# Performance work log

Hardware: AMD Instinct MI355X
Metric: run time of the kernel (lower is better)

Reference implementation:

```python
import jax, jax.numpy as jnp
import numpy as np

B, S, D = 24, 512, 512
H, HS, HSEL = 8, 1, 2
DK = D // H
DFF = 2048
NQ, NPID = 1000, 5000
NB = 2
NL = 3 * NB  # blocks_1 (NB) + blocks_2 (2*NB)
FC1, FC2 = 512, 256


def setup_inputs():
    key = jax.random.key(0)
    ks = jax.random.split(key, 32)
    def w(k, shape, scale=0.02):
        return jax.random.normal(k, shape, dtype=jnp.float32) * scale
    inp = {}
    inp['q_data'] = jax.random.randint(ks[0], (B, S), 0, NQ + 1)
    inp['target'] = jax.random.randint(ks[1], (B, S), 0, 2)
    inp['pid_data'] = jax.random.randint(ks[2], (B, S), 0, NPID + 1)
    # embedding tables (padding_idx=0 -> zero row)
    inp['q_embed_tab'] = w(ks[3], (NQ + 1, D)).at[0].set(0.0)
    inp['qa_embed_tab'] = w(ks[4], (3, D)).at[0].set(0.0)
    inp['q_diff_tab'] = w(ks[5], (NQ + 1, D)).at[0].set(0.0)
    inp['qa_diff_tab'] = w(ks[6], (2 * NQ + 1, D)).at[0].set(0.0)
    inp['pid_diff_tab'] = w(ks[7], (NPID + 1, 1)).at[0].set(0.0)
    # stacked per-layer transformer params, leading dim NL
    inp['Wq'] = w(ks[8], (NL, D, D)); inp['bq'] = jnp.zeros((NL, D), jnp.float32)
    inp['Wv'] = w(ks[9], (NL, D, D)); inp['bv'] = jnp.zeros((NL, D), jnp.float32)
    inp['Wg'] = w(ks[10], (NL, D, H - HS))  # router, no bias
    inp['Wo'] = w(ks[11], (NL, D, D)); inp['bo'] = jnp.zeros((NL, D), jnp.float32)
    inp['ln1_g'] = jnp.ones((NL, D), jnp.float32); inp['ln1_b'] = jnp.zeros((NL, D), jnp.float32)
    inp['W1'] = w(ks[12], (NL, D, DFF)); inp['b1'] = jnp.zeros((NL, DFF), jnp.float32)
    inp['W2'] = w(ks[13], (NL, DFF, D)); inp['b2'] = jnp.zeros((NL, D), jnp.float32)
    inp['ln2_g'] = jnp.ones((NL, D), jnp.float32); inp['ln2_b'] = jnp.zeros((NL, D), jnp.float32)
    # output MLP
    inp['ow1'] = w(ks[14], (2 * D, FC1)); inp['ob1'] = jnp.zeros((FC1,), jnp.float32)
    inp['ow2'] = w(ks[15], (FC1, FC2)); inp['ob2'] = jnp.zeros((FC2,), jnp.float32)
    inp['ow3'] = w(ks[16], (FC2, 1)); inp['ob3'] = jnp.zeros((1,), jnp.float32)
    return inp


def _ln(x, g, b, eps=1e-5):
    m = x.mean(-1, keepdims=True)
    v = ((x - m) ** 2).mean(-1, keepdims=True)
    return (x - m) * jax.lax.rsqrt(v + eps) * g + b


def _moh_attn(xq, xv, strict, Wq, bq, Wv, bv, Wg, Wo, bo):
    b, s, d = xq.shape
    ql = xq @ Wq + bq            # [b,s,D]; kq_same=True so k == q
    vl = xv @ Wv + bv
    q = ql.reshape(b, s, H, DK).transpose(0, 2, 1, 3)   # [b,H,s,dk]
    v = vl.reshape(b, s, H, DK).transpose(0, 2, 1, 3)
    scores = jnp.einsum('bhid,bhjd->bhij', q, q) / np.float32(np.sqrt(DK))
    i = jnp.arange(s)[:, None]
    j = jnp.arange(s)[None, :]
    allowed = (j < i) if strict else (j <= i)
    scores = jnp.where(allowed, scores, jnp.float32(-1e9))
    scores = scores.at[:, :, 0, :].set(0.0)  # pad_zero row -> uniform softmax
    # dynamic per-token head routing on the query projection
    gates = jax.nn.softmax(ql @ Wg, axis=-1)             # [b,s,H-HS]
    idx = jax.lax.top_k(gates, HSEL)[1]                  # [b,s,HSEL]
    dyn_mask = jax.nn.one_hot(idx, H - HS, dtype=gates.dtype).sum(-2)
    dyn_scores = gates * dyn_mask
    rmask = jnp.concatenate([jnp.ones((b, s, HS), gates.dtype), dyn_scores], -1).mean(1)  # [b,H]
    attn = jax.nn.softmax(scores, axis=-1)
    ctx = jnp.einsum('bhij,bhjd->bhid', attn, v) * rmask[:, :, None, None]
    ctx = ctx.transpose(0, 2, 1, 3).reshape(b, s, d)
    return ctx @ Wo + bo


def _block(xq, xv, strict, p):
    a = _moh_attn(xq, xv, strict, *p[:7])
    x = _ln(xq + a, p[7], p[8])
    f = jnp.maximum(x @ p[9] + p[10], 0.0) @ p[11] + p[12]
    return _ln(x + f, p[13], p[14])


def reference(q_data, target, pid_data, q_embed_tab, qa_embed_tab, q_diff_tab,
              qa_diff_tab, pid_diff_tab, Wq, bq, Wv, bv, Wg, Wo, bo,
              ln1_g, ln1_b, W1, b1, W2, b2, ln2_g, ln2_b,
              ow1, ob1, ow2, ob2, ow3, ob3):
    # Rasch-style embeddings (separate_qa=False, n_pid>0)
    q_emb = q_embed_tab[q_data]
    qa_emb = qa_embed_tab[target] + q_emb
    pid_emb = pid_diff_tab[pid_data]          # [B,S,1]
    qd = q_diff_tab[q_data]
    q_emb = q_emb + pid_emb * qd
    qa_emb = qa_emb + pid_emb * (qa_diff_tab[target] + qd)
    stacks = (Wq, bq, Wv, bv, Wg, Wo, bo, ln1_g, ln1_b, W1, b1, W2, b2, ln2_g, ln2_b)
    def P(i):
        return tuple(a[i] for a in stacks)
    y, x = qa_emb, q_emb
    for i in range(NB):                       # blocks_1: mask=1 (causal incl self)
        y = _block(y, y, False, P(i))
    flag = True
    for jj in range(2 * NB):                  # blocks_2: alternate self / cross-with-y
        i = NB + jj
        if flag:
            x = _block(x, x, False, P(i)); flag = False
        else:
            x = _block(x, y, True, P(i)); flag = True
    h = jnp.concatenate([x, q_emb], -1)       # [B,S,2D]
    h = jnp.maximum(h @ ow1 + ob1, 0.0)
    h = jnp.maximum(h @ ow2 + ob2, 0.0)
    return jax.nn.sigmoid((h @ ow3 + ob3)[..., 0])  # [B,S]
```

## Files before the change

### kernel.cpp

```cpp
#include <hip/hip_runtime.h>
#include <math.h>

typedef unsigned short u16;
typedef unsigned int   u32;
typedef __attribute__((ext_vector_type(8))) short short8;
typedef __attribute__((ext_vector_type(4))) float f32x4;

#define Bb 24
#define Ss 512
#define Dd 512
#define DFFf 2048

__device__ __forceinline__ u16 f2b(float f) {
  u32 u = __float_as_uint(f);
  u32 r = (u + 0x7fffu + ((u >> 16) & 1u)) >> 16;
  return (u16)r;
}
__device__ __forceinline__ float b2f(u32 h) { return __uint_as_float(h << 16); }
__device__ __forceinline__ void cvt8(uint4 p, float* d) {
  d[0]=b2f(p.x&0xffffu); d[1]=b2f(p.x>>16);
  d[2]=b2f(p.y&0xffffu); d[3]=b2f(p.y>>16);
  d[4]=b2f(p.z&0xffffu); d[5]=b2f(p.z>>16);
  d[6]=b2f(p.w&0xffffu); d[7]=b2f(p.w>>16);
}

__global__ __launch_bounds__(256) void trans_kernel(
    const float* __restrict__ src, u16* __restrict__ dst, int K, int N,
    int dstLayer, int rowBase)
{
  __shared__ float t[32][33];
  int n0 = blockIdx.x*32, k0 = blockIdx.y*32;
  const float* s = src + (size_t)blockIdx.z*K*N;
  u16* d = dst + (size_t)blockIdx.z*dstLayer;
  int c = threadIdx.x & 31, r = threadIdx.x >> 5;
  #pragma unroll
  for (int rr=r; rr<32; rr+=8) t[rr][c] = s[(size_t)(k0+rr)*N + n0 + c];
  __syncthreads();
  #pragma unroll
  for (int rr=r; rr<32; rr+=8) d[(size_t)(rowBase + n0+rr)*K + k0 + c] = f2b(t[c][rr]);
}

__global__ __launch_bounds__(256) void embed_kernel(
    const int* __restrict__ q_data, const int* __restrict__ target, const int* __restrict__ pid_data,
    const float* __restrict__ q_tab, const float* __restrict__ qa_tab,
    const float* __restrict__ qd_tab, const float* __restrict__ qad_tab,
    const float* __restrict__ pid_tab,
    float* __restrict__ xb, float* __restrict__ yb,
    u16* __restrict__ qebf, u16* __restrict__ ybf)
{
  int t = blockIdx.x;
  int qi = q_data[t], tg = target[t], pi = pid_data[t];
  float pd = pid_tab[pi];
  const float* qe  = q_tab  + (size_t)qi*Dd;
  const float* qa  = qa_tab + (size_t)tg*Dd;
  const float* qd  = qd_tab + (size_t)qi*Dd;
  const float* qad = qad_tab+ (size_t)tg*Dd;
  size_t base = (size_t)t*Dd;
  for (int d = threadIdx.x; d < Dd; d += 256) {
    float e = qe[d], dv = qd[d];
    float qv  = e + pd*dv;
    float qav = qa[d] + e + pd*(qad[d] + dv);
    xb[base+d] = qv;  qebf[base+d] = f2b(qv);
    yb[base+d] = qav; ybf[base+d]  = f2b(qav);
  }
}

__global__ __launch_bounds__(256) void embed_x_kernel(
    const int* __restrict__ q_data, const int* __restrict__ pid_data,
    const float* __restrict__ q_tab, const float* __restrict__ qd_tab,
    const float* __restrict__ pid_tab, float* __restrict__ xb)
{
  int t = blockIdx.x;
  int qi = q_data[t], pi = pid_data[t];
  float pd = pid_tab[pi];
  const float* qe = q_tab + (size_t)qi*Dd;
  const float* qd = qd_tab + (size_t)qi*Dd;
  size_t base = (size_t)t*Dd;
  for (int d = threadIdx.x; d < Dd; d += 256)
    xb[base+d] = qe[d] + pd*qd[d];
}

__global__ __launch_bounds__(256) void gemm_bf16_kernel(
    const u16* __restrict__ A, const u16* __restrict__ A2,
    const u16* __restrict__ Wt,
    const float* __restrict__ bias, const float* __restrict__ bias2,
    float* __restrict__ Cf, u16* __restrict__ Cb, u16* __restrict__ Cb2,
    int M, int N, int K, int ldA, int ldw, int act, int nsplit, float* rinit)
{
  __shared__ u16 As[2][128*32];
  __shared__ u16 Bs[2][128*32];
  if (rinit && blockIdx.x==0 && blockIdx.y==0 && threadIdx.x < 192)
    rinit[threadIdx.x] = ((threadIdx.x & 7)==0) ? 1.f : 0.f;
  int bm = blockIdx.y*128, bn = blockIdx.x*128;
  int wv = threadIdx.x >> 6, lane = threadIdx.x & 63;
  int wm = (wv & 1)*64, wn = (wv >> 1)*64;

  const char* gAa[2]; const char* gAb[2]; const char* gB[2];
  u32 ldsOff[2];
  #pragma unroll
  for (int t=0; t<2; t++) {
    int flat = wv*128 + t*64 + lane;
    int row = flat >> 2, cb = (flat & 3)*16;
    gAa[t] = (const char*)A + ((size_t)(bm+row)*ldA)*2 + cb;
    gAb[t] = A2 ? ((const char*)A2 + ((size_t)(bm+row)*ldA)*2 + cb) : gAa[t];
    gB[t]  = (const char*)Wt + ((size_t)(bn+row)*ldw)*2 + cb;
    ldsOff[t] = (u32)(wv*128 + t*64)*16;
  }
  int selLim = A2 ? 512 : 0x7fffffff;
  int kmask  = A2 ? 511 : 0x7fffffff;

  f32x4 acc[4][4];
  #pragma unroll
  for (int i=0;i<4;i++)
    #pragma unroll
    for (int j=0;j<4;j++) acc[i][j] = (f32x4){0.f,0.f,0.f,0.f};

  int mrow = lane & 15, quad = lane >> 4;

  auto stage = [&](int kt, int buf) {
    int k0 = kt*32;
    size_t offA = (size_t)(k0 & kmask)*2;
    size_t offB = (size_t)k0*2;
    #pragma unroll
    for (int t=0; t<2; t++) {
      const char* sa = ((k0 < selLim) ? gAa[t] : gAb[t]) + offA;
      __builtin_amdgcn_global_load_lds(
          (const __attribute__((address_space(1))) void*)sa,
          (__attribute__((address_space(3))) void*)((char*)As[buf] + ldsOff[t]), 16, 0, 0);
      __builtin_amdgcn_global_load_lds(
          (const __attribute__((address_space(1))) void*)(gB[t] + offB),
          (__attribute__((address_space(3))) void*)((char*)Bs[buf] + ldsOff[t]), 16, 0, 0);
    }
  };

  int nk = K >> 5;
  stage(0, 0);
  for (int t=0; t<nk; t++) {
    __syncthreads();
    if (t+1 < nk) stage(t+1, (t+1)&1);
    const u16* Ab = As[t&1];
    const u16* Bbuf = Bs[t&1];
    short8 af[4], bfr[4];
    #pragma unroll
    for (int i=0;i<4;i++) {
      af[i]  = *(const short8*)(Ab   + (wm + i*16 + mrow)*32 + quad*8);
      bfr[i] = *(const short8*)(Bbuf + (wn + i*16 + mrow)*32 + quad*8);
    }
    #pragma unroll
    for (int i=0;i<4;i++)
      #pragma unroll
      for (int j=0;j<4;j++)
        acc[i][j] = __builtin_amdgcn_mfma_f32_16x16x32_bf16(af[i], bfr[j], acc[i][j], 0, 0, 0);
  }

  int hi = (bias2 != nullptr) && (bn >= nsplit);
  const float* bse = hi ? bias2 : bias;
  u16* outb = hi ? Cb2 : Cb;
  int cb0 = hi ? nsplit : 0;
  int strideOut = bias2 ? nsplit : N;

  #pragma unroll
  for (int i=0;i<4;i++) {
    #pragma unroll
    for (int r=0;r<4;r++) {
      int row = bm + wm + i*16 + quad*4 + r;
      #pragma unroll
      for (int j=0;j<4;j++) {
        int col = bn + wn + j*16 + mrow;
        float v = acc[i][j][r];
        if (bse) v += bse[col - cb0];
        if (act) v = fmaxf(v, 0.f);
        if (Cf)   Cf[(size_t)row*strideOut + col - cb0] = v;
        if (outb) outb[(size_t)row*strideOut + col - cb0] = f2b(v);
      }
    }
  }
}

__device__ __forceinline__ float blockSum256(float v) {
  __shared__ float sh[4];
  #pragma unroll
  for (int o=32;o;o>>=1) v += __shfl_down(v,o);
  if ((threadIdx.x & 63)==0) sh[threadIdx.x>>6]=v;
  __syncthreads();
  float r = sh[0]+sh[1]+sh[2]+sh[3];
  __syncthreads();
  return r;
}

__global__ __launch_bounds__(256) void add_ln_kernel(
    const float* __restrict__ xa, const u16* __restrict__ xbb,
    const float* __restrict__ g, const float* __restrict__ bta,
    float* __restrict__ outf, u16* __restrict__ outb)
{
  size_t base = (size_t)blockIdx.x*Dd;
  int tid = threadIdx.x;
  float v0 = xa[base+tid]     + b2f(xbb[base+tid]);
  float v1 = xa[base+tid+256] + b2f(xbb[base+tid+256]);
  float mean = blockSum256(v0+v1) * (1.f/512.f);
  float d0 = v0-mean, d1 = v1-mean;
  float var = blockSum256(d0*d0 + d1*d1) * (1.f/512.f);
  float inv = rsqrtf(var + 1e-5f);
  float r0 = d0*inv*g[tid]     + bta[tid];
  float r1 = d1*inv*g[tid+256] + bta[tid+256];
  outf[base+tid]     = r0; outb[base+tid]     = f2b(r0);
  outf[base+tid+256] = r1; outb[base+tid+256] = f2b(r1);
}

__global__ __launch_bounds__(64) void router_kernel(
    const u16* __restrict__ ql, const float* __restrict__ Wg, float* __restrict__ rmask)
{
  int b = blockIdx.x >> 3, seg = blockIdx.x & 7;
  int lane = threadIdx.x;
  int s = seg*64 + lane;
  const u16* q = ql + ((size_t)b*Ss + s)*Dd;
  float lg[7];
  #pragma unroll
  for (int k=0;k<7;k++) lg[k]=0.f;
  for (int d0=0; d0<Dd; d0+=8) {
    uint4 p = *(const uint4*)(q+d0);
    float qa[8]; cvt8(p, qa);
    #pragma unroll
    for (int i=0;i<8;i++)
      #pragma unroll
      for (int k=0;k<7;k++) lg[k] += qa[i]*Wg[(d0+i)*7+k];
  }
  float mx = lg[0];
  #pragma unroll
  for (int k=1;k<7;k++) mx = fmaxf(mx, lg[k]);
  float sum = 0.f, gt[7];
  #pragma unroll
  for (int k=0;k<7;k++){ gt[k]=__expf(lg[k]-mx); sum+=gt[k]; }
  float invs = 1.f/sum;
  #pragma unroll
  for (int k=0;k<7;k++) gt[k]*=invs;
  int i1=0; float v1=gt[0];
  #pragma unroll
  for (int k=1;k<7;k++) if (gt[k]>v1){v1=gt[k]; i1=k;}
  int i2=-1; float v2=-1e30f;
  #pragma unroll
  for (int k=0;k<7;k++) if (k!=i1 && gt[k]>v2){v2=gt[k]; i2=k;}
  #pragma unroll
  for (int k=0;k<7;k++) {
    float d = (k==i1 || k==i2) ? gt[k] : 0.f;
    #pragma unroll
    for (int o=32;o;o>>=1) d += __shfl_down(d,o);
    if (lane==0) atomicAdd(&rmask[b*8 + 1 + k], d * (1.f/512.f));
  }
}

__global__ __launch_bounds__(256) void attn_mfma_kernel(
    const u16* __restrict__ ql, const u16* __restrict__ vl,
    const float* __restrict__ rmask, u16* __restrict__ ctx, int strict)
{
  __shared__ u16 Ks[64*64];
  __shared__ u16 Vts[64*64];
  __shared__ u16 Pw[4][32*72];
  int qt = blockIdx.x;
  int b = blockIdx.y >> 3, h = blockIdx.y & 7;
  int tid = threadIdx.x;
  int wv = tid >> 6, lane = tid & 63;
  int mrow = lane & 15, quad = lane >> 4;

  int rowbase[2];
  rowbase[0] = qt*128 + wv*16;
  rowbase[1] = rowbase[0] + 64;

  short8 qf[2][2];
  #pragma unroll
  for (int i=0;i<2;i++)
    #pragma unroll
    for (int kf=0;kf<2;kf++)
      qf[i][kf] = *(const short8*)(ql + (size_t)(b*Ss + rowbase[i] + mrow)*Dd + h*64 + kf*32 + quad*8);

  f32x4 O[2][4];
  f32x4 L[2];
  #pragma unroll
  for (int i=0;i<2;i++) {
    L[i] = (f32x4){0.f,0.f,0.f,0.f};
    #pragma unroll
    for (int df=0;df<4;df++) O[i][df] = (f32x4){0.f,0.f,0.f,0.f};
  }
  short8 ones;
  #pragma unroll
  for (int z=0;z<8;z++) ones[z] = (short)0x3F80;

  int nt = 2*qt + 2;
  for (int t=0; t<nt; t++) {
    int j0 = t*64;
    __syncthreads();
    #pragma unroll
    for (int s2=0; s2<2; s2++) {
      int c = s2*256 + tid;
      int r = c >> 3, o = c & 7;
      uint4 kq = *(const uint4*)(ql + (size_t)(b*Ss + j0 + r)*Dd + h*64 + o*8);
      *(uint4*)(Ks + r*64 + ((o ^ (r&7))*8)) = kq;
    }
    {
      int j = tid & 63, d0 = (tid >> 6) * 16;
      const u16* vp = vl + (size_t)(b*Ss + j0 + j)*Dd + h*64 + d0;
      uint4 va = *(const uint4*)vp;
      uint4 vb = *(const uint4*)(vp + 8);
      u16 vals[16];
      vals[0]=(u16)va.x;  vals[1]=(u16)(va.x>>16);
      vals[2]=(u16)va.y;  vals[3]=(u16)(va.y>>16);
      vals[4]=(u16)va.z;  vals[5]=(u16)(va.z>>16);
      vals[6]=(u16)va.w;  vals[7]=(u16)(va.w>>16);
      vals[8]=(u16)vb.x;  vals[9]=(u16)(vb.x>>16);
      vals[10]=(u16)vb.y; vals[11]=(u16)(vb.y>>16);
      vals[12]=(u16)vb.z; vals[13]=(u16)(vb.z>>16);
      vals[14]=(u16)vb.w; vals[15]=(u16)(vb.w>>16);
      int jg = j >> 3, jo = j & 7;
      #pragma unroll
      for (int dd=0; dd<16; dd++) {
        int d = d0 + dd;
        Vts[d*64 + ((jg ^ (d&7))*8) + jo] = vals[dd];
      }
    }
    __syncthreads();

    f32x4 s[2][4];
    #pragma unroll
    for (int n=0;n<4;n++) {
      int r = n*16 + mrow, rs = r & 7;
      short8 kb0 = *(const short8*)(Ks + r*64 + ((quad  ^ rs))*8);
      short8 kb1 = *(const short8*)(Ks + r*64 + (((quad+4) ^ rs))*8);
      #pragma unroll
      for (int i=0;i<2;i++) {
        f32x4 a = (f32x4){0.f,0.f,0.f,0.f};
        a = __builtin_amdgcn_mfma_f32_16x16x32_bf16(qf[i][0], kb0, a, 0, 0, 0);
        a = __builtin_amdgcn_mfma_f32_16x16x32_bf16(qf[i][1], kb1, a, 0, 0, 0);
        s[i][n] = a;
      }
    }
    #pragma unroll
    for (int i=0;i<2;i++) {
      int rb = rowbase[i] + quad*4 - strict;
      #pragma unroll
      for (int n=0;n<4;n++) {
        int j = j0 + n*16 + mrow;
        #pragma unroll
        for (int r=0;r<4;r++) {
          float v = s[i][n][r]*0.125f;
          float p = (j <= rb + r) ? __expf(fminf(v, 60.f)) : 0.f;
          Pw[wv][(i*16 + quad*4 + r)*72 + n*16 + mrow] = f2b(p);
        }
      }
    }
    asm volatile("s_waitcnt lgkmcnt(0)" ::: "memory");
    short8 pf[2][2];
    #pragma unroll
    for (int pi=0; pi<2; pi++)
      #pragma unroll
      for (int kk=0; kk<2; kk++)
        pf[pi][kk] = *(const short8*)(&Pw[wv][(pi*16 + mrow)*72 + kk*32 + quad*8]);
    #pragma unroll
    for (int i=0;i<2;i++) {
      L[i] = __builtin_amdgcn_mfma_f32_16x16x32_bf16(pf[i][0], ones, L[i], 0, 0, 0);
      L[i] = __builtin_amdgcn_mfma_f32_16x16x32_bf16(pf[i][1], ones, L[i], 0, 0, 0);
    }
    #pragma unroll
    for (int df=0; df<4; df++) {
      int r = df*16 + mrow, rs = r & 7;
      short8 vb0 = *(const short8*)(Vts + r*64 + ((quad ^ rs))*8);
      short8 vb1 = *(const short8*)(Vts + r*64 + (((quad+4) ^ rs))*8);
      #pragma unroll
      for (int i=0;i<2;i++) {
        O[i][df] = __builtin_amdgcn_mfma_f32_16x16x32_bf16(pf[i][0], vb0, O[i][df], 0, 0, 0);
        O[i][df] = __builtin_amdgcn_mfma_f32_16x16x32_bf16(pf[i][1], vb1, O[i][df], 0, 0, 0);
      }
    }
  }

  float rm = rmask[b*8+h];
  #pragma unroll
  for (int i=0;i<2;i++) {
    #pragma unroll
    for (int r=0;r<4;r++) {
      int grow = rowbase[i] + quad*4 + r;
      if (grow != 0) {
        float sc = rm / L[i][r];
        u16* op = ctx + (size_t)(b*Ss + grow)*Dd + h*64 + mrow;
        #pragma unroll
        for (int df=0;df<4;df++)
          op[df*16] = f2b(O[i][df][r]*sc);
      }
    }
  }
}

__global__ __launch_bounds__(64) void attn_row0_kernel(
    const u16* __restrict__ vl, const float* __restrict__ rmask, u16* __restrict__ ctx)
{
  int b = blockIdx.x >> 3, h = blockIdx.x & 7;
  int d = threadIdx.x;
  float s = 0.f;
  for (int j=0;j<Ss;j++) s += b2f(vl[((size_t)b*Ss+j)*Dd + h*64 + d]);
  ctx[(size_t)b*Ss*Dd + h*64 + d] = f2b(s * rmask[b*8+h] * (1.f/512.f));
}

__global__ __launch_bounds__(256) void head_kernel(
    const float* __restrict__ m2, const float* __restrict__ ow3, const float* __restrict__ ob3,
    float* __restrict__ out)
{
  int wave = threadIdx.x >> 6, lane = threadIdx.x & 63;
  int t = blockIdx.x*4 + wave;
  const float* r = m2 + (size_t)t*256;
  float s = 0.f;
  #pragma unroll
  for (int c=0;c<4;c++) s += r[lane + c*64] * ow3[lane + c*64];
  #pragma unroll
  for (int o=32;o;o>>=1) s += __shfl_down(s,o);
  if (lane==0) out[t] = 1.f/(1.f + __expf(-(s + ob3[0])));
}

static inline void gemmb(const u16* A, const u16* A2, const u16* Wt,
                         const float* b1_, const float* b2_,
                         float* Cf, u16* Cb, u16* Cb2,
                         int M, int N, int K, int ldA, int ldw, int act, int nsplit,
                         float* rinit, hipStream_t s) {
  gemm_bf16_kernel<<<dim3(N/128, M/128), 256, 0, s>>>(
      A, A2, Wt, b1_, b2_, Cf, Cb, Cb2, M, N, K, ldA, ldw, act, nsplit, rinit);
}

extern "C" void kernel_launch(void* const* d_in, const int* in_sizes, int n_in,
                              void* d_out, int out_size, void* d_ws, size_t ws_size,
                              hipStream_t stream) {
  const int*   q_data  = (const int*)d_in[0];
  const int*   target  = (const int*)d_in[1];
  const int*   pid_data= (const int*)d_in[2];
  const float* q_tab   = (const float*)d_in[3];
  const float* qa_tab  = (const float*)d_in[4];
  const float* qd_tab  = (const float*)d_in[5];
  const float* qad_tab = (const float*)d_in[6];
  const float* pid_tab = (const float*)d_in[7];
  const float* Wq = (const float*)d_in[8];
  const float* bq = (const float*)d_in[9];
  const float* Wv = (const float*)d_in[10];
  const float* bv = (const float*)d_in[11];
  const float* Wg = (const float*)d_in[12];
  const float* Wo = (const float*)d_in[13];
  const float* bo = (const float*)d_in[14];
  const float* ln1_g = (const float*)d_in[15];
  const float* ln1_b = (const float*)d_in[16];
  const float* W1 = (const float*)d_in[17];
  const float* b1 = (const float*)d_in[18];
  const float* W2 = (const float*)d_in[19];
  const float* b2 = (const float*)d_in[20];
  const float* ln2_g = (const float*)d_in[21];
  const float* ln2_b = (const float*)d_in[22];
  const float* ow1 = (const float*)d_in[23];
  const float* ob1 = (const float*)d_in[24];
  const float* ow2 = (const float*)d_in[25];
  const float* ob2 = (const float*)d_in[26];
  const float* ow3 = (const float*)d_in[27];
  const float* ob3 = (const float*)d_in[28];

  const size_t F = (size_t)Bb*Ss*Dd;
  float* ws = (float*)d_ws;
  float* Ax = ws;
  float* By = ws + F;
  float* Dt = ws + 2*F;
  u16* us = (u16*)(ws + 3*F);
  u16* Gy = us;
  u16* Hc = us + F;
  u16* Iq = us + 2*F;
  u16* Fx = us + 3*F;
  u16* Jq = us + 4*F;
  u16* Kv = us + 5*F;
  u16* Ma = us + 6*F;
  u16* wb = us + 7*F;
  u16* FFh = Fx;

  u16* WqvT = wb;
  u16* WoT  = WqvT + (size_t)6*1024*512;
  u16* W1T  = WoT  + (size_t)6*512*512;
  u16* W2T  = W1T  + (size_t)6*2048*512;
  u16* o1T  = W2T  + (size_t)6*512*2048;
  u16* o2T  = o1T  + (size_t)512*1024;
  float* rmaskb = (float*)(o2T + (size_t)256*512);

  const int M = Bb*Ss;

  trans_kernel<<<dim3(16,16,6), 256, 0, stream>>>(Wq, WqvT, 512, 512, 1024*512, 0);
  trans_kernel<<<dim3(16,16,6), 256, 0, stream>>>(Wv, WqvT, 512, 512, 1024*512, 512);
  trans_kernel<<<dim3(16,16,6), 256, 0, stream>>>(Wo, WoT, 512, 512, 512*512, 0);
  trans_kernel<<<dim3(64,16,6), 256, 0, stream>>>(W1, W1T, 512, 2048, 2048*512, 0);
  trans_kernel<<<dim3(16,64,6), 256, 0, stream>>>(W2, W2T, 2048, 512, 512*2048, 0);
  trans_kernel<<<dim3(16,32,1), 256, 0, stream>>>(ow1, o1T, 1024, 512, 0, 0);
  trans_kernel<<<dim3(8,16,1),  256, 0, stream>>>(ow2, o2T, 512, 256, 0, 0);

  embed_kernel<<<M, 256, 0, stream>>>(q_data, target, pid_data, q_tab, qa_tab,
                                      qd_tab, qad_tab, pid_tab, Ax, By, Iq, Gy);

  for (int l=0; l<6; l++) {
    int strict = (l==3||l==5) ? 1 : 0;
    const u16* Qbf  = (l<2) ? Gy : (l==2 ? Iq : Fx);
    const u16* Xvbf = (l<2) ? Gy : ((l==3||l==5) ? Gy : (l==4 ? Fx : Iq));
    float* Qf   = (l<2) ? By : Ax;
    float* x1f  = (l<2) ? Ax : By;
    u16*   Qout = (l<2) ? Gy : Fx;

    if (l==2)
      embed_x_kernel<<<M, 256, 0, stream>>>(q_data, pid_data, q_tab, qd_tab, pid_tab, Ax);

    const u16* WqvL = WqvT + (size_t)l*1024*512;
    if (!strict) {
      gemmb(Qbf, nullptr, WqvL, bq + l*512, bv + l*512, nullptr, Jq, Kv,
            M, 1024, 512, 512, 512, 0, 512, rmaskb, stream);
    } else {
      gemmb(Qbf,  nullptr, WqvL,                   bq + l*512, nullptr, nullptr, Jq, nullptr,
            M, 512, 512, 512, 512, 0, 512, rmaskb, stream);
      gemmb(Xvbf, nullptr, WqvL + (size_t)512*512, bv + l*512, nullptr, nullptr, Kv, nullptr,
            M, 512, 512, 512, 512, 0, 512, nullptr, stream);
    }
    router_kernel<<<Bb*8, 64, 0, stream>>>(Jq, Wg + (size_t)l*512*7, rmaskb);
    attn_mfma_kernel<<<dim3(4, Bb*8), 256, 0, stream>>>(Jq, Kv, rmaskb, Hc, strict);
    attn_row0_kernel<<<Bb*8, 64, 0, stream>>>(Kv, rmaskb, Hc);
    gemmb(Hc, nullptr, WoT + (size_t)l*512*512, bo + l*512, nullptr, nullptr, Ma, nullptr,
          M, 512, 512, 512, 512, 0, 512, nullptr, stream);
    add_ln_kernel<<<M, 256, 0, stream>>>(Qf, Ma, ln1_g + l*512, ln1_b + l*512, x1f, Hc);
    gemmb(Hc, nullptr, W1T + (size_t)l*2048*512, b1 + l*2048, nullptr,
          nullptr, FFh, nullptr, M, 2048, 512, 512, 512, 1, 2048, nullptr, stream);
    gemmb(FFh, nullptr, W2T + (size_t)l*512*2048, b2 + l*512, nullptr,
          nullptr, (u16*)Dt, nullptr, M, 512, 2048, 2048, 2048, 0, 512, nullptr, stream);
    add_ln_kernel<<<M, 256, 0, stream>>>(x1f, (u16*)Dt, ln2_g + l*512, ln2_b + l*512, Qf, Qout);
  }

  gemmb(Fx, Iq, o1T, ob1, nullptr, nullptr, Jq, nullptr,
        M, 512, 1024, 512, 1024, 1, 512, nullptr, stream);
  gemmb(Jq, nullptr, o2T, ob2, nullptr, (float*)Kv, nullptr, nullptr,
        M, 256, 512, 512, 512, 1, 256, nullptr, stream);
  head_kernel<<<M/4, 256, 0, stream>>>((float*)Kv, ow3, ob3, (float*)d_out);
}
```

Baseline: 2.081 ms.

## Triple-buffer GEMM LDS pipeline and fold row-0 attention into attention kernel

The bf16 GEMM moves from double to triple LDS buffering. It prefetches two K-tiles ahead and uses explicit vmcnt waits plus s_barrier instead of __syncthreads, so global loads overlap more with MFMA work. Separately, the row-0 mean-of-V computation becomes an extra block column of the attention kernel, using 256 threads split into four segments with an LDS reduction. This removes one kernel launch per layer. In exchange the GEMM uses more LDS per block, which may lower occupancy, and its correctness depends on the hand-written vmcnt counts.

```diff
diff --git a/kernel.cpp b/kernel.cpp
--- a/kernel.cpp
+++ b/kernel.cpp
@@ -87,8 +87,8 @@
     float* __restrict__ Cf, u16* __restrict__ Cb, u16* __restrict__ Cb2,
     int M, int N, int K, int ldA, int ldw, int act, int nsplit, float* rinit)
 {
-  __shared__ u16 As[2][128*32];
-  __shared__ u16 Bs[2][128*32];
+  __shared__ u16 As[3][128*32];
+  __shared__ u16 Bs[3][128*32];
   if (rinit && blockIdx.x==0 && blockIdx.y==0 && threadIdx.x < 192)
     rinit[threadIdx.x] = ((threadIdx.x & 7)==0) ? 1.f : 0.f;
   int bm = blockIdx.y*128, bn = blockIdx.x*128;
@@ -135,17 +135,23 @@
 
   int nk = K >> 5;
   stage(0, 0);
+  stage(1, 1);
   for (int t=0; t<nk; t++) {
-    __syncthreads();
-    if (t+1 < nk) stage(t+1, (t+1)&1);
-    const u16* Ab = As[t&1];
-    const u16* Bbuf = Bs[t&1];
+    if (t+1 < nk) {
+      asm volatile("s_waitcnt vmcnt(4)\ns_barrier" ::: "memory");
+    } else {
+      asm volatile("s_waitcnt vmcnt(0)\ns_barrier" ::: "memory");
+    }
+    int buf = t % 3;
+    const u16* Ab   = As[buf];
+    const u16* Bbuf = Bs[buf];
     short8 af[4], bfr[4];
     #pragma unroll
     for (int i=0;i<4;i++) {
       af[i]  = *(const short8*)(Ab   + (wm + i*16 + mrow)*32 + quad*8);
       bfr[i] = *(const short8*)(Bbuf + (wn + i*16 + mrow)*32 + quad*8);
     }
+    if (t+2 < nk) stage(t+2, (t+2) % 3);
     #pragma unroll
     for (int i=0;i<4;i++)
       #pragma unroll
@@ -259,6 +265,23 @@
   int qt = blockIdx.x;
   int b = blockIdx.y >> 3, h = blockIdx.y & 7;
   int tid = threadIdx.x;
+
+  if (qt == 4) {
+    int d = tid & 63, seg = tid >> 6;
+    const u16* vp = vl + (size_t)(b*Ss + seg*128)*Dd + h*64 + d;
+    float s = 0.f;
+    #pragma unroll 4
+    for (int j=0; j<128; j++) s += b2f(vp[(size_t)j*Dd]);
+    float* red = (float*)Ks;
+    red[seg*64 + d] = s;
+    __syncthreads();
+    if (seg == 0) {
+      float tot = red[d] + red[64+d] + red[128+d] + red[192+d];
+      ctx[(size_t)b*Ss*Dd + h*64 + d] = f2b(tot * rmask[b*8+h] * (1.f/512.f));
+    }
+    return;
+  }
+
   int wv = tid >> 6, lane = tid & 63;
   int mrow = lane & 15, quad = lane >> 4;
 
@@ -387,16 +410,6 @@
       }
     }
   }
-}
-
-__global__ __launch_bounds__(64) void attn_row0_kernel(
-    const u16* __restrict__ vl, const float* __restrict__ rmask, u16* __restrict__ ctx)
-{
-  int b = blockIdx.x >> 3, h = blockIdx.x & 7;
-  int d = threadIdx.x;
-  float s = 0.f;
-  for (int j=0;j<Ss;j++) s += b2f(vl[((size_t)b*Ss+j)*Dd + h*64 + d]);
-  ctx[(size_t)b*Ss*Dd + h*64 + d] = f2b(s * rmask[b*8+h] * (1.f/512.f));
 }
 
 __global__ __launch_bounds__(256) void head_kernel(
@@ -515,8 +528,7 @@
             M, 512, 512, 512, 512, 0, 512, nullptr, stream);
     }
     router_kernel<<<Bb*8, 64, 0, stream>>>(Jq, Wg + (size_t)l*512*7, rmaskb);
-    attn_mfma_kernel<<<dim3(4, Bb*8), 256, 0, stream>>>(Jq, Kv, rmaskb, Hc, strict);
-    attn_row0_kernel<<<Bb*8, 64, 0, stream>>>(Kv, rmaskb, Hc);
+    attn_mfma_kernel<<<dim3(5, Bb*8), 256, 0, stream>>>(Jq, Kv, rmaskb, Hc, strict);
     gemmb(Hc, nullptr, WoT + (size_t)l*512*512, bo + l*512, nullptr, nullptr, Ma, nullptr,
           M, 512, 512, 512, 512, 0, 512, nullptr, stream);
     add_ln_kernel<<<M, 256, 0, stream>>>(Qf, Ma, ln1_g + l*512, ln1_b + l*512, x1f, Hc);
```

After: 1.939 ms. -6.8%, faster.
